# Performance work log

Hardware: AMD Instinct MI355X
Metric: run time of the kernel (lower is better)

Reference implementation:

```python
import jax, jax.numpy as jnp
import numpy as np

B, S, D = 2, 2048, 1024
H, KV, HD = 16, 4, 64
F, E, K = 2816, 8, 2
EPS = 1e-6

def setup_inputs() -> dict:
    key = jax.random.key(0)
    ks = jax.random.split(key, 9)
    def rn(k, shape, std=0.02):
        return jax.random.normal(k, shape, dtype=jnp.float32) * std
    inv_freq = 1.0 / (10000.0 ** (jnp.arange(0, HD, 2, dtype=jnp.float32) / HD))
    freqs = jnp.arange(S, dtype=jnp.float32)[:, None] * inv_freq[None, :]
    emb = jnp.concatenate([freqs, freqs], axis=-1)  # [S, HD]
    return {
        'hidden_states': rn(ks[0], (B, S, D), 1.0),
        'ln1_w': jnp.ones((D,), jnp.float32),
        'ln2_w': jnp.ones((D,), jnp.float32),
        'q_w': rn(ks[1], (H * HD, D)), 'q_b': jnp.zeros((H * HD,), jnp.float32),
        'k_w': rn(ks[2], (KV * HD, D)), 'k_b': jnp.zeros((KV * HD,), jnp.float32),
        'v_w': rn(ks[3], (KV * HD, D)), 'v_b': jnp.zeros((KV * HD,), jnp.float32),
        'o_w': rn(ks[4], (D, H * HD)),
        'router_w': rn(ks[5], (E, D), 0.01),
        'gate_w': rn(ks[6], (E, D, F)),
        'up_w': rn(ks[7], (E, D, F)),
        'down_w': rn(ks[8], (E, F, D)),
        'cos': jnp.cos(emb), 'sin': jnp.sin(emb),
    }

def _rmsnorm(x, w):
    v = jnp.mean(jnp.square(x.astype(jnp.float32)), axis=-1, keepdims=True)
    return (x.astype(jnp.float32) * jax.lax.rsqrt(v + EPS)).astype(x.dtype) * w

def _rotate_half(x):
    h = x.shape[-1] // 2
    return jnp.concatenate([-x[..., h:], x[..., :h]], axis=-1)

def reference(hidden_states, ln1_w, ln2_w, q_w, q_b, k_w, k_b, v_w, v_b, o_w, router_w, gate_w, up_w, down_w, cos, sin):
    # --- attention block (RMSNorm -> Qwen2Attention with RoPE+GQA -> residual) ---
    residual = hidden_states
    h = _rmsnorm(hidden_states, ln1_w)
    q = (h @ q_w.T + q_b).reshape(B, S, H, HD).transpose(0, 2, 1, 3)   # [B,H,S,HD]
    k = (h @ k_w.T + k_b).reshape(B, S, KV, HD).transpose(0, 2, 1, 3)  # [B,KV,S,HD]
    v = (h @ v_w.T + v_b).reshape(B, S, KV, HD).transpose(0, 2, 1, 3)
    c = cos[None, None]; s = sin[None, None]
    q = q * c + _rotate_half(q) * s
    k = k * c + _rotate_half(k) * s
    rep = H // KV
    k = jnp.repeat(k, rep, axis=1)
    v = jnp.repeat(v, rep, axis=1)
    scores = jnp.einsum('bhqd,bhkd->bhqk', q, k) / jnp.sqrt(jnp.float32(HD))
    causal = jnp.tril(jnp.ones((S, S), dtype=bool))
    scores = jnp.where(causal[None, None], scores, jnp.finfo(scores.dtype).min)
    attn = jax.nn.softmax(scores, axis=-1)
    ctx = jnp.einsum('bhqk,bhkd->bhqd', attn, v).transpose(0, 2, 1, 3).reshape(B, S, H * HD)
    x = ctx @ o_w.T + residual
    # --- MoE block (RMSNorm -> router -> expert SwiGLU MLPs -> combine -> residual) ---
    residual = x
    t = _rmsnorm(x, ln2_w).reshape(-1, D)  # [T, D], T = B*S
    logits = t @ router_w.T                # [T, E]
    probs = jax.nn.softmax(logits, axis=-1)
    topk_p, topk_i = jax.lax.top_k(probs, K)
    topk_p = topk_p / jnp.sum(topk_p, axis=-1, keepdims=True)
    # dispatch/combine weights [T,E]: vectorized form of the per-token scatter loop
    w = jnp.sum(jax.nn.one_hot(topk_i, E, dtype=t.dtype) * topk_p[..., None], axis=1)
    aux_loss = jnp.mean(E * jnp.square(jnp.mean(probs, axis=0)))
    out = jnp.zeros_like(t)
    for e in range(E):  # fixed small expert loop
        he = jax.nn.silu(t @ gate_w[e]) * (t @ up_w[e])
        out = out + (he @ down_w[e]) * w[:, e:e + 1]
    x = out.reshape(B, S, D) + residual
    return (x, aux_loss)
```

## Files before the change

### kernel.cpp

```cpp
#include <hip/hip_runtime.h>
#include <hip/hip_bf16.h>

#define DEVI __device__ __forceinline__

typedef float f32x4 __attribute__((ext_vector_type(4)));
typedef _Float16 f16x8 __attribute__((ext_vector_type(8)));
typedef short s16x8 __attribute__((ext_vector_type(8)));
typedef unsigned int u32;

constexpr int Bc = 2, Sc = 2048, Dc = 1024, Hc = 16, KVc = 4, HDc = 64, Fc = 2816, Ec = 8;
constexpr int Tc = Bc * Sc;
constexpr int QKVN = Hc * HDc + 2 * KVc * HDc;
constexpr int CAP = Tc * 2 + Ec * 128;
constexpr float LO_SCALE = 1024.0f;
constexpr float LO_INV = 1.0f / 1024.0f;

DEVI f32x4 mfma16(f16x8 a, f16x8 b, f32x4 c) {
    return __builtin_amdgcn_mfma_f32_16x16x32_f16(a, b, c, 0, 0, 0);
}
DEVI f32x4 mfma16(s16x8 a, s16x8 b, f32x4 c) {
    return __builtin_amdgcn_mfma_f32_16x16x32_bf16(a, b, c, 0, 0, 0);
}

DEVI void gll16(const void *g, void *l) {
    __builtin_amdgcn_global_load_lds(
        (const __attribute__((address_space(1))) u32 *)g,
        (__attribute__((address_space(3))) u32 *)l, 16, 0, 0);
}

DEVI u32 pack2(_Float16 a, _Float16 b) {
    union { _Float16 h[2]; u32 u; } t;
    t.h[0] = a; t.h[1] = b;
    return t.u;
}

template <int N> DEVI void wait_vm() {
    if constexpr (N == 0) asm volatile("s_waitcnt vmcnt(0)" ::: "memory");
    else if constexpr (N == 4) asm volatile("s_waitcnt vmcnt(4)" ::: "memory");
    else if constexpr (N == 6) asm volatile("s_waitcnt vmcnt(6)" ::: "memory");
    else if constexpr (N == 8) asm volatile("s_waitcnt vmcnt(8)" ::: "memory");
    else if constexpr (N == 12) asm volatile("s_waitcnt vmcnt(12)" ::: "memory");
}

template <typename VT> struct FragT;
template <> struct FragT<_Float16> { using type = f16x8; };
template <> struct FragT<__hip_bfloat16> { using type = s16x8; };

struct GemmP {
    const void *Ah, *Al;
    const void *Bh, *Bl, *Bh2;
    long lda, ldb, bExp, K;
    const int *poff, *gidx;
    const float *bias, *resid, *bw;
    float *outF, *outF2;
    __hip_bfloat16 *outBF;
    _Float16 *rQh, *rQl, *rKh, *rKl;
    long ldc;
    int epi;
};

template <typename VT, bool SPLIT, bool GATHER, bool GU, int BN, bool XSWZ = false, int NBUF = 2>
__global__ __launch_bounds__(256, SPLIT ? 3 : ((GU && BN == 128) ? 2 : 4)) void gemm_k(GemmP p) {
    constexpr int BM = 128;
    constexpr int NJ = BN / 32;
    constexpr bool HAS2 = SPLIT || GU;
    constexpr int ACH = SPLIT ? 1024 : 512;
    constexpr int BCH = BN * 4;
    constexpr int NB = HAS2 ? 2 : 1;
    constexpr int TOT = ACH + NB * BCH;
    constexpr int NCH = TOT / 256;
    constexpr int BUFVT = TOT * 8;
    constexpr int AOFF2 = 4096;
    constexpr int BOFF = ACH * 8;
    constexpr int B2OFF = (ACH + BCH) * 8;
    __shared__ __align__(16) VT s[NBUF][BUFVT];
    const int tid = threadIdx.x, lane = tid & 63;
    const int wid = tid >> 6, wm = wid >> 1, wn = wid & 1;
    const int x = lane & 15, hi = lane >> 4;
    int mb = (int)blockIdx.x;
    if constexpr (XSWZ) mb = (mb & 7) * ((int)gridDim.x >> 3) + (mb >> 3);
    long m0 = (long)mb * BM, n0 = (long)blockIdx.y * BN;
    int e = 0;
    if (p.poff) {
        int tot = p.poff[Ec];
        if (m0 >= tot) return;
        while (m0 >= p.poff[e + 1]) ++e;
    }

    const VT *gs[NCH];
    int chd[NCH];
#pragma unroll
    for (int i = 0; i < NCH; ++i) {
        int ch = tid + i * 256;
        chd[i] = ch;
        if (ch < ACH) {
            int slab = ch >> 9, local = ch & 511;
            int r = local >> 2, c = local & 3;
            int cs = c ^ ((r >> 1) & 3);
            long ar = m0 + r;
            if (GATHER) ar = p.gidx[ar];
            const VT *mat = (SPLIT && slab == 1) ? (const VT *)p.Al : (const VT *)p.Ah;
            gs[i] = mat + ar * p.lda + cs * 8;
        } else {
            int idx = ch - ACH;
            int which = idx / BCH, local = idx % BCH;
            int r = local >> 2, c = local & 3;
            int cs = c ^ ((r >> 1) & 3);
            const VT *bmat = (which == 0) ? (const VT *)p.Bh
                           : (SPLIT ? (const VT *)p.Bl : (const VT *)p.Bh2);
            gs[i] = bmat + (long)e * p.bExp + (n0 + r) * p.ldb + cs * 8;
        }
    }

    f32x4 acc[4][NJ];
    f32x4 acc2[HAS2 ? 4 : 1][HAS2 ? NJ : 1];
#pragma unroll
    for (int i = 0; i < 4; ++i)
#pragma unroll
        for (int j = 0; j < NJ; ++j) {
            acc[i][j] = (f32x4){0.f, 0.f, 0.f, 0.f};
            if constexpr (HAS2) acc2[i][j] = (f32x4){0.f, 0.f, 0.f, 0.f};
        }

    using F8 = typename FragT<VT>::type;
    const int KT = (int)(p.K / 32);
    auto stageTo = [&](int kt, int b) {
#pragma unroll
        for (int i = 0; i < NCH; ++i)
            gll16(gs[i] + (long)kt * 32, &s[b][(size_t)chd[i] * 8]);
    };

    stageTo(0, 0);
    if (KT > 1) stageTo(1, 1 % NBUF);
    if (NBUF == 3 && KT > 2) stageTo(2, 2 % NBUF);

    int cur = 0;
    for (int kt = 0; kt < KT; ++kt) {
        const int rem = KT - 1 - kt;
        if (rem >= NBUF - 1) wait_vm<(NBUF - 1) * NCH>();
        else if (NBUF == 3 && rem == 1) wait_vm<NCH>();
        else wait_vm<0>();
        __builtin_amdgcn_sched_barrier(0);
        __builtin_amdgcn_s_barrier();
        __builtin_amdgcn_sched_barrier(0);

        F8 afh[4], afl[SPLIT ? 4 : 1];
#pragma unroll
        for (int mi = 0; mi < 4; ++mi) {
            int ar = wm * 64 + mi * 16 + x;
            int ad = (ar * 4 + (hi ^ ((ar >> 1) & 3))) * 8;
            afh[mi] = *(const F8 *)&s[cur][ad];
            if constexpr (SPLIT) afl[mi] = *(const F8 *)&s[cur][AOFF2 + ad];
        }
        __builtin_amdgcn_s_setprio(1);
#pragma unroll
        for (int nj = 0; nj < NJ; ++nj) {
            int br = wn * (BN / 2) + nj * 16 + x;
            int bd = (br * 4 + (hi ^ ((br >> 1) & 3))) * 8;
            F8 bfh = *(const F8 *)&s[cur][BOFF + bd];
            F8 bf2;
            if constexpr (HAS2) bf2 = *(const F8 *)&s[cur][B2OFF + bd];
#pragma unroll
            for (int mi = 0; mi < 4; ++mi) {
                acc[mi][nj] = mfma16(afh[mi], bfh, acc[mi][nj]);
                if constexpr (SPLIT) {
                    acc2[mi][nj] = mfma16(afh[mi], bf2, acc2[mi][nj]);
                    acc2[mi][nj] = mfma16(afl[mi], bfh, acc2[mi][nj]);
                }
                if constexpr (GU) acc2[mi][nj] = mfma16(afh[mi], bf2, acc2[mi][nj]);
            }
        }
        __builtin_amdgcn_s_setprio(0);

        asm volatile("s_waitcnt lgkmcnt(0)" ::: "memory");
        __builtin_amdgcn_sched_barrier(0);
        __builtin_amdgcn_s_barrier();
        __builtin_amdgcn_sched_barrier(0);
        if (kt + NBUF < KT) stageTo(kt + NBUF, cur);
        cur = (cur + 1 == NBUF) ? 0 : cur + 1;
    }

    if (SPLIT && p.epi == 6) {
        float *sEpi = (float *)&s[0][0];
#pragma unroll
        for (int mi = 0; mi < 4; ++mi)
#pragma unroll
            for (int nj = 0; nj < NJ; ++nj)
#pragma unroll
                for (int r = 0; r < 4; ++r) {
                    int rl = wm * 64 + mi * 16 + hi * 4 + r;
                    int cl = wn * (BN / 2) + nj * 16 + x;
                    float v = fmaf(acc2[mi][nj][r], LO_INV, acc[mi][nj][r]) + p.bias[n0 + cl];
                    sEpi[rl * 64 + cl] = v;
                }
        __syncthreads();
        const bool isV = (n0 >= 1280);
        const bool isK = (n0 >= 1024) && !isV;
#pragma unroll
        for (int mi = 0; mi < 4; ++mi)
#pragma unroll
            for (int nj = 0; nj < NJ; ++nj)
#pragma unroll
                for (int r = 0; r < 4; ++r) {
                    int rl = wm * 64 + mi * 16 + hi * 4 + r;
                    int cl = wn * (BN / 2) + nj * 16 + x;
                    long row = m0 + rl;
                    float xv = sEpi[rl * 64 + cl];
                    if (isV) {
                        p.outF[row * 256 + (n0 - 1280) + cl] = xv;
                    } else {
                        int spos = (int)(row & (Sc - 1));
                        float xp = sEpi[rl * 64 + (cl ^ 32)];
                        float cs = p.resid[spos * 64 + cl];
                        float sn = p.bw[spos * 64 + cl];
                        float o = xv * cs + ((cl < 32) ? -xp : xp) * sn;
                        _Float16 hv = (_Float16)o;
                        _Float16 lo = (_Float16)((o - (float)hv) * LO_SCALE);
                        if (isK) {
                            long off = row * 256 + (n0 - 1024) + cl;
                            p.rKh[off] = hv; p.rKl[off] = lo;
                        } else {
                            long off = row * 1024 + n0 + cl;
                            p.rQh[off] = hv; p.rQl[off] = lo;
                        }
                    }
                }
        return;
    }

#pragma unroll
    for (int mi = 0; mi < 4; ++mi)
#pragma unroll
        for (int nj = 0; nj < NJ; ++nj)
#pragma unroll
            for (int r = 0; r < 4; ++r) {
                long row = m0 + wm * 64 + mi * 16 + hi * 4 + r;
                long col = n0 + wn * (BN / 2) + nj * 16 + x;
                float v = acc[mi][nj][r];
                if constexpr (GU) {
                    float u = acc2[mi][nj][r];
                    float he = v / (1.f + __expf(-v)) * u;
                    p.outBF[row * p.ldc + col] = __float2bfloat16(he);
                } else {
                    if constexpr (SPLIT) v = fmaf(acc2[mi][nj][r], LO_INV, v);
                    switch (p.epi) {
                    case 0: p.outF[row * p.ldc + col] = v + p.bias[col]; break;
                    case 2: {
                        float o = v + p.resid[row * p.ldc + col];
                        p.outF[row * p.ldc + col] = o;
                        p.outF2[row * p.ldc + col] = o;
                    } break;
                    case 5:
                        p.outF[row * p.ldc + col] = v * p.bw[row];
                        break;
                    }
                }
            }
}

__global__ __launch_bounds__(256) void combine_k(const float *__restrict__ scat,
        const int *__restrict__ tok_slot, float *__restrict__ out) {
    const long tok = blockIdx.x;
    const int c = threadIdx.x * 4;
    const long s0 = tok_slot[tok * 2], s1 = tok_slot[tok * 2 + 1];
    f32x4 a = *(const f32x4 *)(scat + s0 * Dc + c);
    f32x4 b = *(const f32x4 *)(scat + s1 * Dc + c);
    f32x4 o = *(const f32x4 *)(out + tok * Dc + c);
#pragma unroll
    for (int j = 0; j < 4; ++j) o[j] += a[j] + b[j];
    *(f32x4 *)(out + tok * Dc + c) = o;
}

__global__ __launch_bounds__(128, 2) void attn_k(
    const _Float16 *__restrict__ qh, const _Float16 *__restrict__ ql,
    const _Float16 *__restrict__ kh, const _Float16 *__restrict__ kl,
    const _Float16 *__restrict__ vTh, const _Float16 *__restrict__ vTl,
    _Float16 *__restrict__ ctxh, _Float16 *__restrict__ ctxl) {
    __shared__ __align__(16) _Float16 kbuf[2][2][32 * 64];
    __shared__ __align__(16) _Float16 vbuf[2][2][64 * 32];
    const int tid = threadIdx.x, lane = tid & 63, wid = tid >> 6;
    const int x = lane & 15, hi = lane >> 4;
    const int pairI = blockIdx.x;
    const int bh = blockIdx.y;
    const int b = bh >> 4, h = bh & 15, kvh = h >> 2;
    const long kRow0 = (long)b * Sc * 256;
    const long vRow0 = (long)(b * 4 + kvh) * 64 * (long)Sc;

    auto stage = [&](int kt, int bufI) {
        if (wid == 0) {
#pragma unroll
            for (int ss = 0; ss < 2; ++ss) {
                const _Float16 *src = ss ? kl : kh;
#pragma unroll
                for (int i = 0; i < 4; ++i) {
                    int kv = 8 * i + (lane >> 3);
                    int cd = (lane & 7) ^ (kv & 7);
                    const _Float16 *g = src + kRow0 + ((long)kt * 32 + kv) * 256 + kvh * 64 + cd * 8;
                    gll16(g, &kbuf[bufI][ss][i * 512]);
                }
            }
        } else {
#pragma unroll
            for (int ss = 0; ss < 2; ++ss) {
                const _Float16 *src = ss ? vTl : vTh;
#pragma unroll
                for (int i = 0; i < 4; ++i) {
                    int d = 16 * i + (lane >> 2);
                    int ckv = (lane & 3) ^ ((d >> 1) & 3);
                    const _Float16 *g = src + vRow0 + (long)d * Sc + (long)kt * 32 + ckv * 8;
                    gll16(g, &vbuf[bufI][ss][i * 512]);
                }
            }
        }
    };

    for (int seg = 0; seg < 2; ++seg) {
        const int qt = seg ? (63 - pairI) : pairI;
        const int q0 = qt * 32;
        const long qtokW = (long)b * Sc + q0 + wid * 16;

        f16x8 qfh[2], qfl[2];
#pragma unroll
        for (int ks = 0; ks < 2; ++ks) {
            long off = (qtokW + x) * (long)Dc + h * 64 + ks * 32 + hi * 8;
            qfh[ks] = *(const f16x8 *)(qh + off);
            qfl[ks] = *(const f16x8 *)(ql + off);
        }
        asm volatile("s_waitcnt vmcnt(0)" ::: "memory");
        __builtin_amdgcn_sched_barrier(0);

        f32x4 o1[4], o2[4];
        float mrow = -3.0e38f, lrow = 0.f;
#pragma unroll
        for (int dj = 0; dj < 4; ++dj) {
            o1[dj] = (f32x4){0.f, 0.f, 0.f, 0.f};
            o2[dj] = (f32x4){0.f, 0.f, 0.f, 0.f};
        }

        const int NT = qt + 1;

        stage(0, 0);
        stage(1, 1);

        for (int kt = 0; kt < NT; ++kt) {
            if (kt + 1 < NT) asm volatile("s_waitcnt vmcnt(8)" ::: "memory");
            else asm volatile("s_waitcnt vmcnt(0)" ::: "memory");
            __builtin_amdgcn_sched_barrier(0);
            __builtin_amdgcn_s_barrier();
            __builtin_amdgcn_sched_barrier(0);
            const int cur = kt & 1;

            f32x4 s1[2], s2[2];
#pragma unroll
            for (int kvs = 0; kvs < 2; ++kvs) {
                s1[kvs] = (f32x4){0.f, 0.f, 0.f, 0.f};
                s2[kvs] = (f32x4){0.f, 0.f, 0.f, 0.f};
            }
            __builtin_amdgcn_s_setprio(1);
#pragma unroll
            for (int ks = 0; ks < 2; ++ks)
#pragma unroll
                for (int kvs = 0; kvs < 2; ++kvs) {
                    int row = kvs * 16 + x;
                    int addr = row * 64 + (((ks * 4 + hi) ^ (row & 7)) << 3);
                    f16x8 kfh = *(const f16x8 *)&kbuf[cur][0][addr];
                    f16x8 kfl = *(const f16x8 *)&kbuf[cur][1][addr];
                    s1[kvs] = mfma16(kfh, qfh[ks], s1[kvs]);
                    s2[kvs] = mfma16(kfl, qfh[ks], s2[kvs]);
                    s2[kvs] = mfma16(kfh, qfl[ks], s2[kvs]);
                }
            __builtin_amdgcn_s_setprio(0);

            const bool diag = (kt == NT - 1);
            const int qpos = q0 + wid * 16 + x;
            float sv[2][4];
#pragma unroll
            for (int kvs = 0; kvs < 2; ++kvs)
#pragma unroll
                for (int r = 0; r < 4; ++r) {
                    float v = fmaf(s2[kvs][r], LO_INV, s1[kvs][r]) * 0.125f;
                    if (diag) {
                        int kvpos = kt * 32 + kvs * 16 + 4 * hi + r;
                        if (kvpos > qpos) v = -3.0e38f;
                    }
                    sv[kvs][r] = v;
                }
            float mx = sv[0][0];
#pragma unroll
            for (int kvs = 0; kvs < 2; ++kvs)
#pragma unroll
                for (int r = 0; r < 4; ++r) mx = fmaxf(mx, sv[kvs][r]);
            mx = fmaxf(mx, __shfl_xor(mx, 16));
            mx = fmaxf(mx, __shfl_xor(mx, 32));
            if (!__all(mx - mrow <= 8.0f)) {
                float mnew = fmaxf(mrow, mx);
                float scl = __expf(mrow - mnew);
                mrow = mnew;
                lrow *= scl;
                float sclr[4];
#pragma unroll
                for (int r = 0; r < 4; ++r) sclr[r] = __shfl(scl, 4 * hi + r);
#pragma unroll
                for (int dj = 0; dj < 4; ++dj)
#pragma unroll
                    for (int r = 0; r < 4; ++r) {
                        o1[dj][r] *= sclr[r];
                        o2[dj][r] *= sclr[r];
                    }
            }
            float pv[2][4];
            float ls = 0.f;
#pragma unroll
            for (int kvs = 0; kvs < 2; ++kvs)
#pragma unroll
                for (int r = 0; r < 4; ++r) {
                    pv[kvs][r] = __expf(sv[kvs][r] - mrow);
                    ls += pv[kvs][r];
                }
            ls += __shfl_xor(ls, 16);
            ls += __shfl_xor(ls, 32);
            lrow += ls;
            u32 Bh0[2], Bh1[2], Bl0[2], Bl1[2];
#pragma unroll
            for (int pr = 0; pr < 2; ++pr) {
                _Float16 a0 = (_Float16)pv[0][2 * pr], a1 = (_Float16)pv[0][2 * pr + 1];
                _Float16 b0 = (_Float16)pv[1][2 * pr], b1 = (_Float16)pv[1][2 * pr + 1];
                Bh0[pr] = pack2(a0, a1);
                Bh1[pr] = pack2(b0, b1);
                _Float16 la0 = (_Float16)((pv[0][2 * pr] - (float)a0) * LO_SCALE);
                _Float16 la1 = (_Float16)((pv[0][2 * pr + 1] - (float)a1) * LO_SCALE);
                _Float16 lb0 = (_Float16)((pv[1][2 * pr] - (float)b0) * LO_SCALE);
                _Float16 lb1 = (_Float16)((pv[1][2 * pr + 1] - (float)b1) * LO_SCALE);
                Bl0[pr] = pack2(la0, la1);
                Bl1[pr] = pack2(lb0, lb1);
            }
            const int srcLow = x + ((lane & 16) ? 32 : 0);
            const int srcHigh = srcLow + 16;
            const bool useB1 = lane >= 32;
            union { u32 u[4]; f16x8 v; } fh, fl;
#pragma unroll
            for (int pr = 0; pr < 2; ++pr) {
                u32 t0 = (u32)__shfl((int)Bh0[pr], srcLow);
                u32 t1 = (u32)__shfl((int)Bh1[pr], srcLow);
                fh.u[pr] = useB1 ? t1 : t0;
                u32 u0 = (u32)__shfl((int)Bh0[pr], srcHigh);
                u32 u1 = (u32)__shfl((int)Bh1[pr], srcHigh);
                fh.u[2 + pr] = useB1 ? u1 : u0;
                u32 s0 = (u32)__shfl((int)Bl0[pr], srcLow);
                u32 s1v = (u32)__shfl((int)Bl1[pr], srcLow);
                fl.u[pr] = useB1 ? s1v : s0;
                u32 w0 = (u32)__shfl((int)Bl0[pr], srcHigh);
                u32 w1 = (u32)__shfl((int)Bl1[pr], srcHigh);
                fl.u[2 + pr] = useB1 ? w1 : w0;
            }
            f16x8 pah = fh.v, pal = fl.v;

            __builtin_amdgcn_s_setprio(1);
#pragma unroll
            for (int dj = 0; dj < 4; ++dj) {
                int d = dj * 16 + x;
                int addr = d * 32 + ((hi ^ ((d >> 1) & 3)) << 3);
                f16x8 vhf = *(const f16x8 *)&vbuf[cur][0][addr];
                f16x8 vlf = *(const f16x8 *)&vbuf[cur][1][addr];
                o1[dj] = mfma16(pah, vhf, o1[dj]);
                o2[dj] = mfma16(pah, vlf, o2[dj]);
                o2[dj] = mfma16(pal, vhf, o2[dj]);
            }
            __builtin_amdgcn_s_setprio(0);

            asm volatile("s_waitcnt lgkmcnt(0)" ::: "memory");
            __builtin_amdgcn_sched_barrier(0);
            __builtin_amdgcn_s_barrier();
            __builtin_amdgcn_sched_barrier(0);
            if (kt + 2 < NT) stage(kt + 2, cur);
        }

        float linv = 1.0f / lrow;
        float lr[4];
#pragma unroll
        for (int r = 0; r < 4; ++r) lr[r] = __shfl(linv, 4 * hi + r);
#pragma unroll
        for (int dj = 0; dj < 4; ++dj)
#pragma unroll
            for (int r = 0; r < 4; ++r) {
                long tok = qtokW + 4 * hi + r;
                float ov = fmaf(o2[dj][r], LO_INV, o1[dj][r]) * lr[r];
                _Float16 hv = (_Float16)ov;
                long off = tok * Dc + h * 64 + dj * 16 + x;
                ctxh[off] = hv;
                ctxl[off] = (_Float16)((ov - (float)hv) * LO_SCALE);
            }
    }
}

__global__ __launch_bounds__(256) void rmsnorm_split_k(const float *__restrict__ x,
        const float *__restrict__ w, _Float16 *__restrict__ oh, _Float16 *__restrict__ ol) {
    const long row = blockIdx.x;
    const int tid = threadIdx.x, lane = tid & 63, wid = tid >> 6;
    f32x4 v = *(const f32x4 *)(x + row * Dc + tid * 4);
    float ss = v[0] * v[0] + v[1] * v[1] + v[2] * v[2] + v[3] * v[3];
#pragma unroll
    for (int off = 1; off < 64; off <<= 1) ss += __shfl_xor(ss, off);
    __shared__ float sw[4];
    if (lane == 0) sw[wid] = ss;
    __syncthreads();
    float inv = 1.0f / sqrtf((sw[0] + sw[1] + sw[2] + sw[3]) * (1.f / Dc) + 1e-6f);
#pragma unroll
    for (int j = 0; j < 4; ++j) {
        float y = v[j] * inv * w[tid * 4 + j];
        _Float16 hv = (_Float16)y;
        oh[row * Dc + tid * 4 + j] = hv;
        ol[row * Dc + tid * 4 + j] = (_Float16)((y - (float)hv) * LO_SCALE);
    }
}

__global__ __launch_bounds__(256) void rmsnorm_router_k(const float *__restrict__ x,
        const float *__restrict__ w, const float *__restrict__ rw,
        __hip_bfloat16 *__restrict__ tb, float *__restrict__ probs,
        int *__restrict__ tok_e, float *__restrict__ tok_w, int *__restrict__ cnt) {
    const long row = blockIdx.x;
    const int tid = threadIdx.x, lane = tid & 63, wid = tid >> 6;
    f32x4 v = *(const f32x4 *)(x + row * Dc + tid * 4);
    float ss = v[0] * v[0] + v[1] * v[1] + v[2] * v[2] + v[3] * v[3];
#pragma unroll
    for (int off = 1; off < 64; off <<= 1) ss += __shfl_xor(ss, off);
    __shared__ float sw[4];
    __shared__ float part[4][8];
    if (lane == 0) sw[wid] = ss;
    __syncthreads();
    float inv = 1.0f / sqrtf((sw[0] + sw[1] + sw[2] + sw[3]) * (1.f / Dc) + 1e-6f);
    float y[4];
#pragma unroll
    for (int j = 0; j < 4; ++j) {
        y[j] = v[j] * inv * w[tid * 4 + j];
        tb[row * Dc + tid * 4 + j] = __float2bfloat16(y[j]);
    }
    float acc[8];
#pragma unroll
    for (int e = 0; e < 8; ++e) {
        f32x4 wv = *(const f32x4 *)(rw + (long)e * Dc + tid * 4);
        acc[e] = y[0] * wv[0] + y[1] * wv[1] + y[2] * wv[2] + y[3] * wv[3];
    }
#pragma unroll
    for (int off = 1; off < 64; off <<= 1)
#pragma unroll
        for (int e = 0; e < 8; ++e) acc[e] += __shfl_xor(acc[e], off);
    if (lane == 0)
#pragma unroll
        for (int e = 0; e < 8; ++e) part[wid][e] = acc[e];
    __syncthreads();
    if (tid == 0) {
        float lg[8];
        float mx = -3.0e38f;
#pragma unroll
        for (int e = 0; e < 8; ++e) {
            lg[e] = part[0][e] + part[1][e] + part[2][e] + part[3][e];
            mx = fmaxf(mx, lg[e]);
        }
        float ex[8], s = 0.f;
#pragma unroll
        for (int e = 0; e < 8; ++e) { ex[e] = expf(lg[e] - mx); s += ex[e]; }
        float invs = 1.f / s;
        int i1 = -1, i2 = -1;
        float p1v = -1.f, p2v = -1.f;
#pragma unroll
        for (int e = 0; e < 8; ++e) {
            float pe = ex[e] * invs;
            probs[row * 8 + e] = pe;
            if (pe > p1v) { i2 = i1; p2v = p1v; i1 = e; p1v = pe; }
            else if (pe > p2v) { i2 = e; p2v = pe; }
        }
        float wsum = p1v + p2v;
        tok_e[row * 2] = i1; tok_e[row * 2 + 1] = i2;
        tok_w[row * 2] = p1v / wsum; tok_w[row * 2 + 1] = p2v / wsum;
        atomicAdd(&cnt[i1], 1);
        atomicAdd(&cnt[i2], 1);
    }
}

__global__ void pack_qkvw_k(const float *__restrict__ qw, const float *__restrict__ kw,
        const float *__restrict__ vw, _Float16 *wh, _Float16 *wl) {
    const long n = (long)QKVN * Dc;
    for (long i = (long)blockIdx.x * 256 + threadIdx.x; i < n; i += (long)gridDim.x * 256) {
        long o = i >> 10;
        int d = (int)(i & 1023);
        float v;
        if (o < 1024) v = qw[o * 1024 + d];
        else if (o < 1280) v = kw[(o - 1024) * 1024 + d];
        else v = vw[(o - 1280) * 1024 + d];
        _Float16 h = (_Float16)v;
        wh[i] = h;
        wl[i] = (_Float16)((v - (float)h) * LO_SCALE);
    }
}

__global__ void split_f16_k(const float *__restrict__ x, _Float16 *hi, _Float16 *lo, long n) {
    for (long i = (long)blockIdx.x * 256 + threadIdx.x; i < n; i += (long)gridDim.x * 256) {
        float v = x[i];
        _Float16 h = (_Float16)v;
        hi[i] = h;
        lo[i] = (_Float16)((v - (float)h) * LO_SCALE);
    }
}

__global__ void pack_bias_k(const float *qb, const float *kb, const float *vb, float *out) {
    int i = blockIdx.x * 256 + threadIdx.x;
    if (i >= QKVN) return;
    out[i] = (i < 1024) ? qb[i] : (i < 1280) ? kb[i - 1024] : vb[i - 1280];
}

__global__ __launch_bounds__(256) void transpose_bf16_k(const float *__restrict__ in,
        __hip_bfloat16 *__restrict__ out, int R, int C) {
    __shared__ float tile[64 * 65];
    const long eo = (long)blockIdx.z * R * C;
    const int r0 = blockIdx.y * 64, c0 = blockIdx.x * 64;
#pragma unroll
    for (int i = 0; i < 16; ++i) {
        int idx = threadIdx.x + i * 256;
        int r = idx >> 6, c = idx & 63;
        tile[r * 65 + c] = in[eo + (long)(r0 + r) * C + (c0 + c)];
    }
    __syncthreads();
#pragma unroll
    for (int i = 0; i < 16; ++i) {
        int idx = threadIdx.x + i * 256;
        int cc = idx >> 6, rr = idx & 63;
        out[eo + (long)(c0 + cc) * R + (r0 + rr)] = __float2bfloat16(tile[rr * 65 + cc]);
    }
}

__global__ __launch_bounds__(256) void vtrans_k(const float *__restrict__ vqf,
        _Float16 *__restrict__ vTh, _Float16 *__restrict__ vTl) {
    __shared__ float tile[64][65];
    const int tok0 = blockIdx.x * 64;
    const int bk = blockIdx.y;
    const int b = bk >> 2, kvh = bk & 3;
#pragma unroll
    for (int it = 0; it < 16; ++it) {
        int idx = it * 256 + threadIdx.x;
        int r = idx >> 6, c = idx & 63;
        tile[r][c] = vqf[((long)b * Sc + tok0 + r) * 256 + kvh * 64 + c];
    }
    __syncthreads();
    const int d = threadIdx.x & 63, ch = threadIdx.x >> 6;
    long orow = ((long)bk * 64 + d) * (long)Sc + tok0 + ch * 16;
    f16x8 oh[2], ol[2];
#pragma unroll
    for (int j = 0; j < 16; ++j) {
        float v = tile[ch * 16 + j][d];
        _Float16 hv = (_Float16)v;
        oh[j >> 3][j & 7] = hv;
        ol[j >> 3][j & 7] = (_Float16)((v - (float)hv) * LO_SCALE);
    }
    *(f16x8 *)(vTh + orow) = oh[0];
    *(f16x8 *)(vTh + orow + 8) = oh[1];
    *(f16x8 *)(vTl + orow) = ol[0];
    *(f16x8 *)(vTl + orow + 8) = ol[1];
}

__global__ __launch_bounds__(1024) void router_p2_k(const int *cnt, const float *probs,
        int *poff, float *aux_out) {
    __shared__ float sd[1024];
    const int tid = threadIdx.x;
    const int e = tid & 7, rs = tid >> 3;
    float s = 0.f;
    for (int r = rs; r < Tc; r += 128) s += probs[(long)r * 8 + e];
    sd[tid] = s;
    __syncthreads();
    for (int st = 64; st >= 1; st >>= 1) {
        if (rs < st) sd[tid] += sd[tid + st * 8];
        __syncthreads();
    }
    if (tid == 0) {
        float a = 0.f;
        for (int ee = 0; ee < 8; ++ee) {
            float m = sd[ee] * (1.f / Tc);
            a += m * m;
        }
        aux_out[0] = a;
        int o = 0;
        poff[0] = 0;
        for (int ee = 0; ee < 8; ++ee) { o += (cnt[ee] + 127) & ~127; poff[ee + 1] = o; }
    }
}

__global__ void router_p3_k(const int *tok_e, const float *tok_w, const int *poff,
        int *cursor, int *btok, float *bw, int *tok_slot) {
    long tok = (long)blockIdx.x * 256 + threadIdx.x;
    if (tok >= Tc) return;
#pragma unroll
    for (int j = 0; j < 2; ++j) {
        int e = tok_e[tok * 2 + j];
        int slot = atomicAdd(&cursor[e], 1);
        btok[poff[e] + slot] = (int)tok;
        bw[poff[e] + slot] = tok_w[tok * 2 + j];
        tok_slot[tok * 2 + j] = poff[e] + slot;
    }
}

__global__ void router_p4_k(const int *poff, const int *cnt, int *btok, float *bw) {
    int s = blockIdx.x * 256 + threadIdx.x;
    if (s >= poff[8]) return;
    int e = 0;
    while (s >= poff[e + 1]) ++e;
    if (s - poff[e] >= cnt[e]) { btok[s] = 0; bw[s] = 0.f; }
}

extern "C" void kernel_launch(void *const *d_in, const int *in_sizes, int n_in,
                              void *d_out, int out_size, void *d_ws, size_t ws_size,
                              hipStream_t stream) {
    (void)in_sizes; (void)n_in;
    const float *hidden = (const float *)d_in[0];
    const float *ln1 = (const float *)d_in[1];
    const float *ln2 = (const float *)d_in[2];
    const float *qw = (const float *)d_in[3];
    const float *qb = (const float *)d_in[4];
    const float *kw = (const float *)d_in[5];
    const float *kb = (const float *)d_in[6];
    const float *vw = (const float *)d_in[7];
    const float *vb = (const float *)d_in[8];
    const float *ow = (const float *)d_in[9];
    const float *rw = (const float *)d_in[10];
    const float *gw = (const float *)d_in[11];
    const float *uw = (const float *)d_in[12];
    const float *dwn = (const float *)d_in[13];
    const float *cosb = (const float *)d_in[14];
    const float *sinb = (const float *)d_in[15];
    float *outx = (float *)d_out;

    char *base = (char *)d_ws;
    size_t off = 0;
    auto alloc = [&](size_t bytes) -> char * {
        char *p = base + off;
        off += (bytes + 255) & ~(size_t)255;
        return p;
    };
    _Float16 *qkvwh = (_Float16 *)alloc((size_t)QKVN * Dc * 2);
    _Float16 *qkvwl = (_Float16 *)alloc((size_t)QKVN * Dc * 2);
    float *qkvb = (float *)alloc(QKVN * 4);
    _Float16 *owh = (_Float16 *)alloc((size_t)Dc * Dc * 2);
    _Float16 *owl = (_Float16 *)alloc((size_t)Dc * Dc * 2);
    __hip_bfloat16 *gateT = (__hip_bfloat16 *)alloc((size_t)Ec * Fc * Dc * 2);
    __hip_bfloat16 *upT = (__hip_bfloat16 *)alloc((size_t)Ec * Fc * Dc * 2);
    __hip_bfloat16 *downT = (__hip_bfloat16 *)alloc((size_t)Ec * Dc * Fc * 2);
    char *U2 = alloc((size_t)Tc * Dc * 4);
    _Float16 *hh = (_Float16 *)U2;
    _Float16 *hl = hh + (size_t)Tc * Dc;
    char *U3 = alloc((size_t)Tc * Dc * 4);
    _Float16 *qhb = (_Float16 *)U3;
    _Float16 *qlb = qhb + (size_t)Tc * Dc;
    float *x1 = (float *)U3;
    _Float16 *khb = (_Float16 *)alloc((size_t)Tc * 256 * 2);
    _Float16 *klb = (_Float16 *)alloc((size_t)Tc * 256 * 2);
    _Float16 *vTh = (_Float16 *)alloc((size_t)Tc * 256 * 2);
    _Float16 *vTl = (_Float16 *)alloc((size_t)Tc * 256 * 2);
    float *scat = (float *)U2;
    _Float16 *ctxh = (_Float16 *)alloc((size_t)Tc * Dc * 2);
    _Float16 *ctxl = (_Float16 *)alloc((size_t)Tc * Dc * 2);
    __hip_bfloat16 *tbf = (__hip_bfloat16 *)alloc((size_t)Tc * Dc * 2);
    float *vqf = (float *)alloc((size_t)Tc * 256 * 4);
    float *probs = (float *)alloc((size_t)Tc * 8 * 4);
    int *tok_e = (int *)alloc((size_t)Tc * 2 * 4);
    float *tok_w = (float *)alloc((size_t)Tc * 2 * 4);
    int *tok_slot = (int *)alloc((size_t)Tc * 2 * 4);
    int *cnt = (int *)alloc(256);
    int *cursor = cnt + 8;
    int *poff = (int *)alloc(256);
    int *btok = (int *)alloc((size_t)CAP * 4);
    float *bwgt = (float *)alloc((size_t)CAP * 4);
    __hip_bfloat16 *gbuf = (__hip_bfloat16 *)alloc((size_t)CAP * Fc * 2);

    if (off > ws_size) {
        hipMemsetAsync(d_out, 0, (size_t)out_size * 4, stream);
        return;
    }

    hipMemsetAsync(cnt, 0, 64, stream);
    pack_qkvw_k<<<1024, 256, 0, stream>>>(qw, kw, vw, qkvwh, qkvwl);
    pack_bias_k<<<(QKVN + 255) / 256, 256, 0, stream>>>(qb, kb, vb, qkvb);
    split_f16_k<<<1024, 256, 0, stream>>>(ow, owh, owl, (long)Dc * Dc);
    transpose_bf16_k<<<dim3(Fc / 64, Dc / 64, Ec), 256, 0, stream>>>(gw, gateT, Dc, Fc);
    transpose_bf16_k<<<dim3(Fc / 64, Dc / 64, Ec), 256, 0, stream>>>(uw, upT, Dc, Fc);
    transpose_bf16_k<<<dim3(Dc / 64, Fc / 64, Ec), 256, 0, stream>>>(dwn, downT, Fc, Dc);
    rmsnorm_split_k<<<Tc, 256, 0, stream>>>(hidden, ln1, hh, hl);

    GemmP g{};
    g.Ah = hh; g.Al = hl; g.Bh = qkvwh; g.Bl = qkvwl;
    g.lda = Dc; g.ldb = Dc; g.bExp = 0; g.K = Dc;
    g.bias = qkvb; g.resid = cosb; g.bw = sinb;
    g.outF = vqf; g.rQh = qhb; g.rQl = qlb; g.rKh = khb; g.rKl = klb;
    g.ldc = QKVN; g.epi = 6;
    gemm_k<_Float16, true, false, false, 64><<<dim3(Tc / 128, QKVN / 64), 256, 0, stream>>>(g);

    vtrans_k<<<dim3(Sc / 64, Bc * KVc), 256, 0, stream>>>(vqf, vTh, vTl);
    attn_k<<<dim3(Sc / 64, Bc * Hc), 128, 0, stream>>>(qhb, qlb, khb, klb, vTh, vTl, ctxh, ctxl);

    GemmP go{};
    go.Ah = ctxh; go.Al = ctxl; go.Bh = owh; go.Bl = owl;
    go.lda = Dc; go.ldb = Dc; go.bExp = 0; go.K = Dc;
    go.resid = hidden; go.outF = x1; go.outF2 = outx; go.ldc = Dc; go.epi = 2;
    gemm_k<_Float16, true, false, false, 64><<<dim3(Tc / 128, Dc / 64), 256, 0, stream>>>(go);

    rmsnorm_router_k<<<Tc, 256, 0, stream>>>(x1, ln2, rw, tbf, probs, tok_e, tok_w, cnt);
    router_p2_k<<<1, 1024, 0, stream>>>(cnt, probs, poff, outx + (long)Tc * Dc);
    router_p3_k<<<Tc / 256, 256, 0, stream>>>(tok_e, tok_w, poff, cursor, btok, bwgt, tok_slot);
    router_p4_k<<<CAP / 256, 256, 0, stream>>>(poff, cnt, btok, bwgt);

    GemmP gg{};
    gg.Ah = tbf; gg.Bh = gateT; gg.Bh2 = upT;
    gg.lda = Dc; gg.ldb = Dc; gg.bExp = (long)Fc * Dc; gg.K = Dc;
    gg.poff = poff; gg.gidx = btok; gg.outBF = gbuf; gg.ldc = Fc;
    gemm_k<__hip_bfloat16, false, true, true, 128, true, 3><<<dim3(CAP / 128, Fc / 128), 256, 0, stream>>>(gg);

    GemmP gd{};
    gd.Ah = gbuf; gd.Bh = downT;
    gd.lda = Fc; gd.ldb = Fc; gd.bExp = (long)Dc * Fc; gd.K = Fc;
    gd.poff = poff; gd.bw = bwgt;
    gd.outF = scat; gd.ldc = Dc; gd.epi = 5;
    gemm_k<__hip_bfloat16, false, false, false, 128, true, 3><<<dim3(CAP / 128, Dc / 128), 256, 0, stream>>>(gd);

    combine_k<<<Tc, 256, 0, stream>>>(scat, tok_slot, outx);
}
```

Baseline: 680.9 us.

## Fuse V transpose and split into QKV GEMM epilogue; drop triple buffering

The QKV GEMM epilogue now transposes the V tile through padded shared memory and writes the fp16 hi/lo transposed V directly. This removes the separate vtrans kernel and the fp32 V intermediate buffer. The shared-memory epilogue stride is padded to 65 to avoid bank conflicts. The GEMM template also drops the NBUF=3 option, so the MoE GEMMs go back to double buffering. That frees LDS and may allow higher occupancy, at the cost of less latency hiding.

```diff
diff --git a/kernel.cpp b/kernel.cpp
--- a/kernel.cpp
+++ b/kernel.cpp
@@ -55,11 +55,12 @@
     float *outF, *outF2;
     __hip_bfloat16 *outBF;
     _Float16 *rQh, *rQl, *rKh, *rKl;
+    _Float16 *rVh, *rVl;
     long ldc;
     int epi;
 };
 
-template <typename VT, bool SPLIT, bool GATHER, bool GU, int BN, bool XSWZ = false, int NBUF = 2>
+template <typename VT, bool SPLIT, bool GATHER, bool GU, int BN, bool XSWZ = false>
 __global__ __launch_bounds__(256, SPLIT ? 3 : ((GU && BN == 128) ? 2 : 4)) void gemm_k(GemmP p) {
     constexpr int BM = 128;
     constexpr int NJ = BN / 32;
@@ -73,7 +74,7 @@
     constexpr int AOFF2 = 4096;
     constexpr int BOFF = ACH * 8;
     constexpr int B2OFF = (ACH + BCH) * 8;
-    __shared__ __align__(16) VT s[NBUF][BUFVT];
+    __shared__ __align__(16) VT s[2][BUFVT];
     const int tid = threadIdx.x, lane = tid & 63;
     const int wid = tid >> 6, wm = wid >> 1, wn = wid & 1;
     const int x = lane & 15, hi = lane >> 4;
@@ -131,18 +132,15 @@
     };
 
     stageTo(0, 0);
-    if (KT > 1) stageTo(1, 1 % NBUF);
-    if (NBUF == 3 && KT > 2) stageTo(2, 2 % NBUF);
-
-    int cur = 0;
+    if (KT > 1) stageTo(1, 1);
+
     for (int kt = 0; kt < KT; ++kt) {
-        const int rem = KT - 1 - kt;
-        if (rem >= NBUF - 1) wait_vm<(NBUF - 1) * NCH>();
-        else if (NBUF == 3 && rem == 1) wait_vm<NCH>();
+        if (kt + 1 < KT) wait_vm<NCH>();
         else wait_vm<0>();
         __builtin_amdgcn_sched_barrier(0);
         __builtin_amdgcn_s_barrier();
         __builtin_amdgcn_sched_barrier(0);
+        const int cur = kt & 1;
 
         F8 afh[4], afl[SPLIT ? 4 : 1];
 #pragma unroll
@@ -176,8 +174,7 @@
         __builtin_amdgcn_sched_barrier(0);
         __builtin_amdgcn_s_barrier();
         __builtin_amdgcn_sched_barrier(0);
-        if (kt + NBUF < KT) stageTo(kt + NBUF, cur);
-        cur = (cur + 1 == NBUF) ? 0 : cur + 1;
+        if (kt + 2 < KT) stageTo(kt + 2, cur);
     }
 
     if (SPLIT && p.epi == 6) {
@@ -191,26 +188,45 @@
                     int rl = wm * 64 + mi * 16 + hi * 4 + r;
                     int cl = wn * (BN / 2) + nj * 16 + x;
                     float v = fmaf(acc2[mi][nj][r], LO_INV, acc[mi][nj][r]) + p.bias[n0 + cl];
-                    sEpi[rl * 64 + cl] = v;
+                    sEpi[rl * 65 + cl] = v;
                 }
         __syncthreads();
         const bool isV = (n0 >= 1280);
-        const bool isK = (n0 >= 1024) && !isV;
-#pragma unroll
-        for (int mi = 0; mi < 4; ++mi)
-#pragma unroll
-            for (int nj = 0; nj < NJ; ++nj)
-#pragma unroll
-                for (int r = 0; r < 4; ++r) {
-                    int rl = wm * 64 + mi * 16 + hi * 4 + r;
-                    int cl = wn * (BN / 2) + nj * 16 + x;
-                    long row = m0 + rl;
-                    float xv = sEpi[rl * 64 + cl];
-                    if (isV) {
-                        p.outF[row * 256 + (n0 - 1280) + cl] = xv;
-                    } else {
+        if (isV) {
+            const int bIdx = (int)(m0 >> 11);
+            const int tok0 = (int)(m0 & (Sc - 1));
+            const int kvh = (int)((n0 - 1280) >> 6);
+            const long vbase = ((long)(bIdx * 4 + kvh) * 64) * (long)Sc;
+#pragma unroll
+            for (int it = 0; it < 4; ++it) {
+                int idx = tid + it * 256;
+                int d = idx >> 4, tch = idx & 15;
+                f16x8 oh, ol;
+#pragma unroll
+                for (int j = 0; j < 8; ++j) {
+                    float v = sEpi[(tch * 8 + j) * 65 + d];
+                    _Float16 hv = (_Float16)v;
+                    oh[j] = hv;
+                    ol[j] = (_Float16)((v - (float)hv) * LO_SCALE);
+                }
+                long orow = vbase + (long)d * Sc + tok0 + tch * 8;
+                *(f16x8 *)(p.rVh + orow) = oh;
+                *(f16x8 *)(p.rVl + orow) = ol;
+            }
+        } else {
+            const bool isK = (n0 >= 1024);
+#pragma unroll
+            for (int mi = 0; mi < 4; ++mi)
+#pragma unroll
+                for (int nj = 0; nj < NJ; ++nj)
+#pragma unroll
+                    for (int r = 0; r < 4; ++r) {
+                        int rl = wm * 64 + mi * 16 + hi * 4 + r;
+                        int cl = wn * (BN / 2) + nj * 16 + x;
+                        long row = m0 + rl;
+                        float xv = sEpi[rl * 65 + cl];
                         int spos = (int)(row & (Sc - 1));
-                        float xp = sEpi[rl * 64 + (cl ^ 32)];
+                        float xp = sEpi[rl * 65 + (cl ^ 32)];
                         float cs = p.resid[spos * 64 + cl];
                         float sn = p.bw[spos * 64 + cl];
                         float o = xv * cs + ((cl < 32) ? -xp : xp) * sn;
@@ -224,7 +240,7 @@
                             p.rQh[off] = hv; p.rQl[off] = lo;
                         }
                     }
-                }
+        }
         return;
     }
 
@@ -627,35 +643,6 @@
         int cc = idx >> 6, rr = idx & 63;
         out[eo + (long)(c0 + cc) * R + (r0 + rr)] = __float2bfloat16(tile[rr * 65 + cc]);
     }
-}
-
-__global__ __launch_bounds__(256) void vtrans_k(const float *__restrict__ vqf,
-        _Float16 *__restrict__ vTh, _Float16 *__restrict__ vTl) {
-    __shared__ float tile[64][65];
-    const int tok0 = blockIdx.x * 64;
-    const int bk = blockIdx.y;
-    const int b = bk >> 2, kvh = bk & 3;
-#pragma unroll
-    for (int it = 0; it < 16; ++it) {
-        int idx = it * 256 + threadIdx.x;
-        int r = idx >> 6, c = idx & 63;
-        tile[r][c] = vqf[((long)b * Sc + tok0 + r) * 256 + kvh * 64 + c];
-    }
-    __syncthreads();
-    const int d = threadIdx.x & 63, ch = threadIdx.x >> 6;
-    long orow = ((long)bk * 64 + d) * (long)Sc + tok0 + ch * 16;
-    f16x8 oh[2], ol[2];
-#pragma unroll
-    for (int j = 0; j < 16; ++j) {
-        float v = tile[ch * 16 + j][d];
-        _Float16 hv = (_Float16)v;
-        oh[j >> 3][j & 7] = hv;
-        ol[j >> 3][j & 7] = (_Float16)((v - (float)hv) * LO_SCALE);
-    }
-    *(f16x8 *)(vTh + orow) = oh[0];
-    *(f16x8 *)(vTh + orow + 8) = oh[1];
-    *(f16x8 *)(vTl + orow) = ol[0];
-    *(f16x8 *)(vTl + orow + 8) = ol[1];
 }
 
 __global__ __launch_bounds__(1024) void router_p2_k(const int *cnt, const float *probs,
@@ -758,7 +745,6 @@
     _Float16 *ctxh = (_Float16 *)alloc((size_t)Tc * Dc * 2);
     _Float16 *ctxl = (_Float16 *)alloc((size_t)Tc * Dc * 2);
     __hip_bfloat16 *tbf = (__hip_bfloat16 *)alloc((size_t)Tc * Dc * 2);
-    float *vqf = (float *)alloc((size_t)Tc * 256 * 4);
     float *probs = (float *)alloc((size_t)Tc * 8 * 4);
     int *tok_e = (int *)alloc((size_t)Tc * 2 * 4);
     float *tok_w = (float *)alloc((size_t)Tc * 2 * 4);
@@ -788,11 +774,10 @@
     g.Ah = hh; g.Al = hl; g.Bh = qkvwh; g.Bl = qkvwl;
     g.lda = Dc; g.ldb = Dc; g.bExp = 0; g.K = Dc;
     g.bias = qkvb; g.resid = cosb; g.bw = sinb;
-    g.outF = vqf; g.rQh = qhb; g.rQl = qlb; g.rKh = khb; g.rKl = klb;
+    g.rQh = qhb; g.rQl = qlb; g.rKh = khb; g.rKl = klb; g.rVh = vTh; g.rVl = vTl;
     g.ldc = QKVN; g.epi = 6;
     gemm_k<_Float16, true, false, false, 64><<<dim3(Tc / 128, QKVN / 64), 256, 0, stream>>>(g);
 
-    vtrans_k<<<dim3(Sc / 64, Bc * KVc), 256, 0, stream>>>(vqf, vTh, vTl);
     attn_k<<<dim3(Sc / 64, Bc * Hc), 128, 0, stream>>>(qhb, qlb, khb, klb, vTh, vTl, ctxh, ctxl);
 
     GemmP go{};
@@ -810,14 +795,14 @@
     gg.Ah = tbf; gg.Bh = gateT; gg.Bh2 = upT;
     gg.lda = Dc; gg.ldb = Dc; gg.bExp = (long)Fc * Dc; gg.K = Dc;
     gg.poff = poff; gg.gidx = btok; gg.outBF = gbuf; gg.ldc = Fc;
-    gemm_k<__hip_bfloat16, false, true, true, 128, true, 3><<<dim3(CAP / 128, Fc / 128), 256, 0, stream>>>(gg);
+    gemm_k<__hip_bfloat16, false, true, true, 128, true><<<dim3(CAP / 128, Fc / 128), 256, 0, stream>>>(gg);
 
     GemmP gd{};
     gd.Ah = gbuf; gd.Bh = downT;
     gd.lda = Fc; gd.ldb = Fc; gd.bExp = (long)Dc * Fc; gd.K = Fc;
     gd.poff = poff; gd.bw = bwgt;
     gd.outF = scat; gd.ldc = Dc; gd.epi = 5;
-    gemm_k<__hip_bfloat16, false, false, false, 128, true, 3><<<dim3(CAP / 128, Dc / 128), 256, 0, stream>>>(gd);
+    gemm_k<__hip_bfloat16, false, false, false, 128, true><<<dim3(CAP / 128, Dc / 128), 256, 0, stream>>>(gd);
 
     combine_k<<<Tc, 256, 0, stream>>>(scat, tok_slot, outx);
 }
```

New measurement: 677.1 us. No clear change (-0.6%).
